# Kernel optimization log

Measured on AMD Instinct MI355X. Metric: run time of the kernel, lower is better.

The kernel has to match this reference:

```python
import jax, jax.numpy as jnp
import numpy as np

B, CQ, CC, COUT, H, W = 32, 256, 3, 256, 32, 32
INTER = CQ // 2
HC, WC = 224, 224
EPS = 1e-5


def setup_inputs() -> dict:
    key = jax.random.key(0)
    ks = jax.random.split(key, 12)
    s = lambda fan_in: 1.0 / np.sqrt(fan_in)
    return {
        "query_feat": jax.random.normal(ks[0], (B, CQ, H, W), jnp.float32),
        "context_feat": jax.random.normal(ks[1], (B, CC, HC, WC), jnp.float32),
        "Wq": jax.random.uniform(ks[2], (INTER, CQ), jnp.float32, -s(CQ), s(CQ)),
        "bq": jax.random.uniform(ks[3], (INTER,), jnp.float32, -s(CQ), s(CQ)),
        "Wk": jax.random.uniform(ks[4], (INTER, CC), jnp.float32, -s(CC), s(CC)),
        "bk": jax.random.uniform(ks[5], (INTER,), jnp.float32, -s(CC), s(CC)),
        "Wv": jax.random.uniform(ks[6], (CQ, CC), jnp.float32, -s(CC), s(CC)),
        "bv": jax.random.uniform(ks[7], (CQ,), jnp.float32, -s(CC), s(CC)),
        "Wp": jax.random.uniform(ks[8], (COUT, CQ), jnp.float32, -s(CQ), s(CQ)),
        "bp": jax.random.uniform(ks[9], (COUT,), jnp.float32, -s(CQ), s(CQ)),
        "gamma": jnp.ones((COUT,), jnp.float32),
        "beta": jnp.zeros((COUT,), jnp.float32),
    }


def _conv1x1(x, Wmat, b):
    # x: [B,Cin,H,W], Wmat: [Cout,Cin] -> [B,Cout,H,W]
    return jnp.einsum("oc,bchw->bohw", Wmat, x) + b[None, :, None, None]


def reference(query_feat, context_feat, Wq, bq, Wk, bk, Wv, bv, Wp, bp, gamma, beta):
    Bn, Cq, Hn, Wn = query_feat.shape
    HWn = Hn * Wn
    # bilinear resize, align_corners=False, no antialias (matches F.interpolate)
    ctx = jax.image.resize(context_feat, (Bn, context_feat.shape[1], Hn, Wn),
                           method="linear", antialias=False)
    q = _conv1x1(query_feat, Wq, bq).reshape(Bn, -1, HWn)   # [B,inter,HW]
    k = _conv1x1(ctx, Wk, bk).reshape(Bn, -1, HWn)          # [B,inter,HW]
    v = _conv1x1(ctx, Wv, bv).reshape(Bn, Cq, HWn)          # [B,Cq,HW]
    scores = jnp.einsum("bci,bcj->bij", q, k)               # [B,HW,HW]
    probs = jax.nn.softmax(scores, axis=-1)
    # attended_v[b,c,i] = sum_j v[b,c,j] * probs[b,i,j]
    attended = jnp.einsum("bcj,bij->bci", v, probs).reshape(Bn, Cq, Hn, Wn)
    fused = _conv1x1(query_feat + attended, Wp, bp)         # [B,Cout,H,W]
    # GroupNorm with 1 group: normalize over (C,H,W) per sample
    mu = jnp.mean(fused, axis=(1, 2, 3), keepdims=True)
    var = jnp.var(fused, axis=(1, 2, 3), keepdims=True)
    normed = (fused - mu) * jax.lax.rsqrt(var + EPS)
    return normed * gamma[None, :, None, None] + beta[None, :, None, None]
```

## Files before the change

kernel.cpp:

```cpp
#include <hip/hip_runtime.h>
#include <hip/hip_bf16.h>

#define WS_M     0
#define WS_G4    1024
#define WS_BSUM  2048
#define WS_BSSQ  2080
#define WS_WPB   2176

typedef __attribute__((ext_vector_type(8))) short short8;
typedef __attribute__((ext_vector_type(4))) float floatx4;

__device__ inline unsigned short f2bf(float x) {
    unsigned u = __float_as_uint(x);
    return (unsigned short)((u + 0x7FFFu + ((u >> 16) & 1u)) >> 16);
}

__global__ __launch_bounds__(256) void sca_pre(
    const float* __restrict__ Wq, const float* __restrict__ bq,
    const float* __restrict__ Wk, const float* __restrict__ bk,
    const float* __restrict__ Wv, const float* __restrict__ bv,
    const float* __restrict__ Wp, const float* __restrict__ bp,
    float* __restrict__ ws)
{
    int tid = threadIdx.x;
    int blk = blockIdx.x;
    if (blk == 0) {
        __shared__ float WkL[384];
        __shared__ float bqL[128];
        if (tid < 128) bqL[tid] = bq[tid];
        for (int idx = tid; idx < 384; idx += 256) WkL[idx] = Wk[idx];
        __syncthreads();
        float m0v = 0.f, m1v = 0.f, m2v = 0.f;
        for (int c0 = 0; c0 < 128; c0 += 16) {
            float q[16];
#pragma unroll
            for (int j = 0; j < 16; ++j) q[j] = Wq[(c0 + j) * 256 + tid];
#pragma unroll
            for (int j = 0; j < 16; ++j) {
                int c = c0 + j;
                m0v = fmaf(WkL[c * 3 + 0], q[j], m0v);
                m1v = fmaf(WkL[c * 3 + 1], q[j], m1v);
                m2v = fmaf(WkL[c * 3 + 2], q[j], m2v);
            }
        }
        ws[WS_M + 0   + tid] = m0v;
        ws[WS_M + 256 + tid] = m1v;
        ws[WS_M + 512 + tid] = m2v;
        if (tid < 3) {
            float s = 0.f;
            for (int c = 0; c < 128; ++c) s = fmaf(WkL[c * 3 + tid], bqL[c], s);
            ws[WS_M + 768 + tid] = s;
        }
        if (tid < 64) ws[WS_BSUM + tid] = 0.f;
    } else if (blk == 1) {
        __shared__ float WvL[768];
        __shared__ float bvL[256];
        for (int idx = tid; idx < 768; idx += 256) WvL[idx] = Wv[idx];
        bvL[tid] = bv[tid];
        __syncthreads();
        float g0 = 0.f, g1 = 0.f, g2 = 0.f, gb = 0.f;
        const float4* wr4 = (const float4*)(Wp + tid * 256);
        for (int c0 = 0; c0 < 64; c0 += 8) {
            float4 wv[8];
#pragma unroll
            for (int j = 0; j < 8; ++j) wv[j] = wr4[c0 + j];
#pragma unroll
            for (int j = 0; j < 8; ++j) {
                int c = (c0 + j) * 4;
                g0 = fmaf(wv[j].x, WvL[(c+0)*3+0], g0); g1 = fmaf(wv[j].x, WvL[(c+0)*3+1], g1); g2 = fmaf(wv[j].x, WvL[(c+0)*3+2], g2); gb = fmaf(wv[j].x, bvL[c+0], gb);
                g0 = fmaf(wv[j].y, WvL[(c+1)*3+0], g0); g1 = fmaf(wv[j].y, WvL[(c+1)*3+1], g1); g2 = fmaf(wv[j].y, WvL[(c+1)*3+2], g2); gb = fmaf(wv[j].y, bvL[c+1], gb);
                g0 = fmaf(wv[j].z, WvL[(c+2)*3+0], g0); g1 = fmaf(wv[j].z, WvL[(c+2)*3+1], g1); g2 = fmaf(wv[j].z, WvL[(c+2)*3+2], g2); gb = fmaf(wv[j].z, bvL[c+2], gb);
                g0 = fmaf(wv[j].w, WvL[(c+3)*3+0], g0); g1 = fmaf(wv[j].w, WvL[(c+3)*3+1], g1); g2 = fmaf(wv[j].w, WvL[(c+3)*3+2], g2); gb = fmaf(wv[j].w, bvL[c+3], gb);
            }
        }
        ((float4*)(ws + WS_G4))[tid] = make_float4(g0, g1, g2, gb + bp[tid]);
    } else {
        int idx = (blk - 2) * 2048 + tid * 8;
        int o = idx >> 8;
        int kt = (tid & 31) >> 2, quad = tid & 3;
        const float4* s = (const float4*)(Wp + idx);
        float4 x0 = s[0], x1 = s[1];
        uint4 v;
        v.x = (unsigned)f2bf(x0.x) | ((unsigned)f2bf(x0.y) << 16);
        v.y = (unsigned)f2bf(x0.z) | ((unsigned)f2bf(x0.w) << 16);
        v.z = (unsigned)f2bf(x1.x) | ((unsigned)f2bf(x1.y) << 16);
        v.w = (unsigned)f2bf(x1.z) | ((unsigned)f2bf(x1.w) << 16);
        int slot = (((o >> 4) * 8 + kt) * 64) + quad * 16 + (o & 15);
        ((uint4*)((unsigned short*)(ws + WS_WPB)))[slot] = v;
    }
}

__global__ __launch_bounds__(256, 2) void sca_fused(const float* __restrict__ Q,
                                                    const float* __restrict__ ctxin,
                                                    float* __restrict__ ws,
                                                    float* __restrict__ out)
{
    __shared__ float Ms[771];
    __shared__ float4 cs[1024];
    __shared__ uint4 QL[2048];
    __shared__ float red[4][16][12];
    __shared__ float4 av4[64];
    __shared__ float4 cps[64];
    int tid = threadIdx.x;
    int blk = blockIdx.x;
    int b  = blk >> 4;
    int i0 = (blk & 15) << 6;

    {
        const float* src = ctxin + (size_t)b * 150528;
        for (int s4 = 0; s4 < 4; ++s4) {
            int j = s4 * 256 + tid;
            int y = j >> 5, x = j & 31;
            int p = (7 * y + 3) * 224 + (7 * x + 3);
            cs[j] = make_float4(src[p], src[p + 50176], src[p + 100352], 0.f);
        }
    }
    for (int idx = tid; idx < 771; idx += 256) Ms[idx] = ws[WS_M + idx];
    __syncthreads();

    int iq = tid & 15, kg = tid >> 4;
    const float* Qp = Q + ((size_t)b << 18) + ((size_t)(kg * 16) << 10) + i0 + iq * 4;
    float a00=0.f,a01=0.f,a02=0.f,a03=0.f;
    float a10=0.f,a11=0.f,a12=0.f,a13=0.f;
    float a20=0.f,a21=0.f,a22=0.f,a23=0.f;
    unsigned pk[4][8];
#pragma unroll
    for (int s = 0; s < 16; ++s) {
        float4 qv = *(const float4*)(Qp + ((size_t)s << 10));
        int c = kg * 16 + s;
        float m0 = Ms[c], m1 = Ms[256 + c], m2 = Ms[512 + c];
        a00 = fmaf(m0, qv.x, a00); a01 = fmaf(m0, qv.y, a01); a02 = fmaf(m0, qv.z, a02); a03 = fmaf(m0, qv.w, a03);
        a10 = fmaf(m1, qv.x, a10); a11 = fmaf(m1, qv.y, a11); a12 = fmaf(m1, qv.z, a12); a13 = fmaf(m1, qv.w, a13);
        a20 = fmaf(m2, qv.x, a20); a21 = fmaf(m2, qv.y, a21); a22 = fmaf(m2, qv.z, a22); a23 = fmaf(m2, qv.w, a23);
        unsigned h0 = f2bf(qv.x), h1 = f2bf(qv.y), h2 = f2bf(qv.z), h3 = f2bf(qv.w);
        int j = s >> 1;
        if (s & 1) {
            pk[0][j] |= h0 << 16; pk[1][j] |= h1 << 16;
            pk[2][j] |= h2 << 16; pk[3][j] |= h3 << 16;
        } else {
            pk[0][j] = h0; pk[1][j] = h1; pk[2][j] = h2; pk[3][j] = h3;
        }
    }
#pragma unroll
    for (int e = 0; e < 4; ++e) {
        int row = iq * 4 + e;
        int sw = (row ^ (row >> 3)) & 7;
#pragma unroll
        for (int h = 0; h < 2; ++h) {
            int g = kg * 2 + h;
            int gs = (g & 24) | ((g ^ sw) & 7);
            QL[row * 32 + gs] =
                make_uint4(pk[e][h*4+0], pk[e][h*4+1], pk[e][h*4+2], pk[e][h*4+3]);
        }
    }
    a00 += __shfl_xor(a00,16); a00 += __shfl_xor(a00,32);
    a01 += __shfl_xor(a01,16); a01 += __shfl_xor(a01,32);
    a02 += __shfl_xor(a02,16); a02 += __shfl_xor(a02,32);
    a03 += __shfl_xor(a03,16); a03 += __shfl_xor(a03,32);
    a10 += __shfl_xor(a10,16); a10 += __shfl_xor(a10,32);
    a11 += __shfl_xor(a11,16); a11 += __shfl_xor(a11,32);
    a12 += __shfl_xor(a12,16); a12 += __shfl_xor(a12,32);
    a13 += __shfl_xor(a13,16); a13 += __shfl_xor(a13,32);
    a20 += __shfl_xor(a20,16); a20 += __shfl_xor(a20,32);
    a21 += __shfl_xor(a21,16); a21 += __shfl_xor(a21,32);
    a22 += __shfl_xor(a22,16); a22 += __shfl_xor(a22,32);
    a23 += __shfl_xor(a23,16); a23 += __shfl_xor(a23,32);
    int lane = tid & 63, w = tid >> 6;
    if (lane < 16) {
        red[w][lane][0]=a00; red[w][lane][1]=a01; red[w][lane][2] =a02; red[w][lane][3] =a03;
        red[w][lane][4]=a10; red[w][lane][5]=a11; red[w][lane][6] =a12; red[w][lane][7] =a13;
        red[w][lane][8]=a20; red[w][lane][9]=a21; red[w][lane][10]=a22; red[w][lane][11]=a23;
    }
    __syncthreads();
    if (tid < 64) {
        int iqq = tid >> 2, e = tid & 3;
        float r0 = red[0][iqq][0+e] + red[1][iqq][0+e] + red[2][iqq][0+e] + red[3][iqq][0+e] + Ms[768];
        float r1 = red[0][iqq][4+e] + red[1][iqq][4+e] + red[2][iqq][4+e] + red[3][iqq][4+e] + Ms[769];
        float r2 = red[0][iqq][8+e] + red[1][iqq][8+e] + red[2][iqq][8+e] + red[3][iqq][8+e] + Ms[770];
        av4[tid] = make_float4(r0, r1, r2, 0.f);
    }
    __syncthreads();

    int m = lane & 15, quad = lane >> 4;
    const short8* Apack = (const short8*)((const unsigned short*)(ws + WS_WPB));
    const short8* QLs = (const short8*)QL;
    floatx4 acc[4][4] = {};
#pragma unroll
    for (int kt = 0; kt < 8; ++kt) {
        short8 af[4], bf[4];
#pragma unroll
        for (int t = 0; t < 4; ++t)
            af[t] = Apack[((w * 4 + t) * 8 + kt) * 64 + lane];
#pragma unroll
        for (int t = 0; t < 4; ++t) {
            int row = t * 16 + m;
            int sw = (row ^ (row >> 3)) & 7;
            int g = kt * 4 + quad;
            int gs = (g & 24) | ((g ^ sw) & 7);
            bf[t] = QLs[row * 32 + gs];
        }
#pragma unroll
        for (int to = 0; to < 4; ++to)
#pragma unroll
            for (int ti = 0; ti < 4; ++ti)
                acc[to][ti] = __builtin_amdgcn_mfma_f32_16x16x32_bf16(
                    af[to], bf[ti], acc[to][ti], 0, 0, 0);
    }

    {
        int qi = tid >> 2, sl = tid & 3;
        float4 a = av4[qi];
        float sh = 6.0f * (fabsf(a.x) + fabsf(a.y) + fabsf(a.z));
        float d = 0.f, s0 = 0.f, s1 = 0.f, s2 = 0.f;
#pragma unroll 4
        for (int jj = 0; jj < 256; ++jj) {
            float4 c = cs[(jj << 2) + sl];
            float sc = fmaf(a.x, c.x, fmaf(a.y, c.y, a.z * c.z));
            float e = __expf(sc - sh);
            d += e;
            s0 = fmaf(e, c.x, s0);
            s1 = fmaf(e, c.y, s1);
            s2 = fmaf(e, c.z, s2);
        }
        d  += __shfl_xor(d, 1);  d  += __shfl_xor(d, 2);
        s0 += __shfl_xor(s0, 1); s0 += __shfl_xor(s0, 2);
        s1 += __shfl_xor(s1, 1); s1 += __shfl_xor(s1, 2);
        s2 += __shfl_xor(s2, 1); s2 += __shfl_xor(s2, 2);
        if (sl == 0) {
            float inv = 1.0f / d;
            cps[qi] = make_float4(s0 * inv, s1 * inv, s2 * inv, 0.f);
        }
    }
    __syncthreads();

    const floatx4* G4 = (const floatx4*)(ws + WS_G4);
    float4 cpv[4];
#pragma unroll
    for (int ti = 0; ti < 4; ++ti) cpv[ti] = cps[ti * 16 + m];
    float lsum = 0.f, lssq = 0.f;
#pragma unroll
    for (int to = 0; to < 4; ++to)
#pragma unroll
        for (int r = 0; r < 4; ++r) {
            int o = w * 64 + to * 16 + quad * 4 + r;
            floatx4 g = G4[o];
            float* orow = out + (((size_t)(b * 256 + o)) << 10) + i0 + m;
#pragma unroll
            for (int ti = 0; ti < 4; ++ti) {
                float v = acc[to][ti][r]
                        + g[0] * cpv[ti].x + g[1] * cpv[ti].y + g[2] * cpv[ti].z + g[3];
                orow[ti * 16] = v;
                lsum += v; lssq = fmaf(v, v, lssq);
            }
        }
#pragma unroll
    for (int off = 32; off > 0; off >>= 1) {
        lsum += __shfl_down(lsum, off);
        lssq += __shfl_down(lssq, off);
    }
    if (lane == 0) {
        atomicAdd(ws + WS_BSUM + b, lsum);
        atomicAdd(ws + WS_BSSQ + b, lssq);
    }
}

__global__ __launch_bounds__(256) void sca_norm(float* __restrict__ out,
                                                const float* __restrict__ ws,
                                                const float* __restrict__ gamma,
                                                const float* __restrict__ beta)
{
    size_t idx = (size_t)blockIdx.x * 256 + threadIdx.x;
    float4 v = ((const float4*)out)[idx];
    size_t base = idx << 2;
    int b = (int)(base >> 18);
    int o = (int)((base >> 10) & 255);
    const float inv_n = 1.0f / 262144.0f;
    float mean = ws[WS_BSUM + b] * inv_n;
    float var  = fmaf(ws[WS_BSSQ + b], inv_n, -mean * mean);
    float rs = rsqrtf(var + 1e-5f);
    float ga = gamma[o] * rs;
    float be = fmaf(-mean, ga, beta[o]);
    v.x = fmaf(v.x, ga, be);
    v.y = fmaf(v.y, ga, be);
    v.z = fmaf(v.z, ga, be);
    v.w = fmaf(v.w, ga, be);
    ((float4*)out)[idx] = v;
}

extern "C" void kernel_launch(void* const* d_in, const int* in_sizes, int n_in,
                              void* d_out, int out_size, void* d_ws, size_t ws_size,
                              hipStream_t stream)
{
    const float* Q     = (const float*)d_in[0];
    const float* ctxf  = (const float*)d_in[1];
    const float* Wq    = (const float*)d_in[2];
    const float* bq    = (const float*)d_in[3];
    const float* Wk    = (const float*)d_in[4];
    const float* bk    = (const float*)d_in[5];
    const float* Wv    = (const float*)d_in[6];
    const float* bv    = (const float*)d_in[7];
    const float* Wp    = (const float*)d_in[8];
    const float* bp    = (const float*)d_in[9];
    const float* gamma = (const float*)d_in[10];
    const float* beta  = (const float*)d_in[11];
    float* ws  = (float*)d_ws;
    float* out = (float*)d_out;

    sca_pre  <<<34,   256, 0, stream>>>(Wq, bq, Wk, bk, Wv, bv, Wp, bp, ws);
    sca_fused<<<512,  256, 0, stream>>>(Q, ctxf, ws, out);
    sca_norm <<<8192, 256, 0, stream>>>(out, ws, gamma, beta);
}
```

Baseline: 173.1 us.

## Parallelize precompute, hoist context gather into pre-kernel, raise fused occupancy

The weight precompute in sca_pre is split across more blocks. The M matrix reduction runs over 4 blocks with shared-memory partial sums, and the G4 projection is folded into the 32 Wp conversion blocks using shuffle reductions. The strided context-subsample gather moves into 128 extra sca_pre blocks that write a compact float4 buffer, so each of the 16 fused blocks per batch no longer re-gathers it with uncoalesced loads. sca_fused switches its context tile to SoA arrays, reuses the red buffer for cps, and targets 3 blocks per CU. sca_norm processes 4 float4s per thread with fewer blocks.

```diff
diff --git a/kernel.cpp b/kernel.cpp
--- a/kernel.cpp
+++ b/kernel.cpp
@@ -6,6 +6,7 @@
 #define WS_BSUM  2048
 #define WS_BSSQ  2080
 #define WS_WPB   2176
+#define WS_CTX   34944
 
 typedef __attribute__((ext_vector_type(8))) short short8;
 typedef __attribute__((ext_vector_type(4))) float floatx4;
@@ -20,21 +21,24 @@
     const float* __restrict__ Wk, const float* __restrict__ bk,
     const float* __restrict__ Wv, const float* __restrict__ bv,
     const float* __restrict__ Wp, const float* __restrict__ bp,
-    float* __restrict__ ws)
+    const float* __restrict__ ctxin, float* __restrict__ ws)
 {
     int tid = threadIdx.x;
     int blk = blockIdx.x;
-    if (blk == 0) {
+    if (blk < 4) {
         __shared__ float WkL[384];
         __shared__ float bqL[128];
+        __shared__ float redM[4][64][3];
+        int o0 = blk << 6;
         if (tid < 128) bqL[tid] = bq[tid];
         for (int idx = tid; idx < 384; idx += 256) WkL[idx] = Wk[idx];
         __syncthreads();
+        int o64 = tid & 63, cg = tid >> 6;
         float m0v = 0.f, m1v = 0.f, m2v = 0.f;
-        for (int c0 = 0; c0 < 128; c0 += 16) {
+        for (int c0 = cg * 32; c0 < cg * 32 + 32; c0 += 16) {
             float q[16];
 #pragma unroll
-            for (int j = 0; j < 16; ++j) q[j] = Wq[(c0 + j) * 256 + tid];
+            for (int j = 0; j < 16; ++j) q[j] = Wq[(c0 + j) * 256 + o0 + o64];
 #pragma unroll
             for (int j = 0; j < 16; ++j) {
                 int c = c0 + j;
@@ -43,39 +47,31 @@
                 m2v = fmaf(WkL[c * 3 + 2], q[j], m2v);
             }
         }
-        ws[WS_M + 0   + tid] = m0v;
-        ws[WS_M + 256 + tid] = m1v;
-        ws[WS_M + 512 + tid] = m2v;
-        if (tid < 3) {
-            float s = 0.f;
-            for (int c = 0; c < 128; ++c) s = fmaf(WkL[c * 3 + tid], bqL[c], s);
-            ws[WS_M + 768 + tid] = s;
-        }
-        if (tid < 64) ws[WS_BSUM + tid] = 0.f;
-    } else if (blk == 1) {
+        redM[cg][o64][0] = m0v; redM[cg][o64][1] = m1v; redM[cg][o64][2] = m2v;
+        __syncthreads();
+        if (tid < 64) {
+            float r0 = redM[0][tid][0] + redM[1][tid][0] + redM[2][tid][0] + redM[3][tid][0];
+            float r1 = redM[0][tid][1] + redM[1][tid][1] + redM[2][tid][1] + redM[3][tid][1];
+            float r2 = redM[0][tid][2] + redM[1][tid][2] + redM[2][tid][2] + redM[3][tid][2];
+            ws[WS_M + 0   + o0 + tid] = r0;
+            ws[WS_M + 256 + o0 + tid] = r1;
+            ws[WS_M + 512 + o0 + tid] = r2;
+        }
+        if (blk == 0) {
+            if (tid < 3) {
+                float s = 0.f;
+                for (int c = 0; c < 128; ++c) s = fmaf(WkL[c * 3 + tid], bqL[c], s);
+                ws[WS_M + 768 + tid] = s;
+            }
+            if (tid < 64) ws[WS_BSUM + tid] = 0.f;
+        }
+    } else if (blk < 36) {
         __shared__ float WvL[768];
         __shared__ float bvL[256];
         for (int idx = tid; idx < 768; idx += 256) WvL[idx] = Wv[idx];
         bvL[tid] = bv[tid];
         __syncthreads();
-        float g0 = 0.f, g1 = 0.f, g2 = 0.f, gb = 0.f;
-        const float4* wr4 = (const float4*)(Wp + tid * 256);
-        for (int c0 = 0; c0 < 64; c0 += 8) {
-            float4 wv[8];
-#pragma unroll
-            for (int j = 0; j < 8; ++j) wv[j] = wr4[c0 + j];
-#pragma unroll
-            for (int j = 0; j < 8; ++j) {
-                int c = (c0 + j) * 4;
-                g0 = fmaf(wv[j].x, WvL[(c+0)*3+0], g0); g1 = fmaf(wv[j].x, WvL[(c+0)*3+1], g1); g2 = fmaf(wv[j].x, WvL[(c+0)*3+2], g2); gb = fmaf(wv[j].x, bvL[c+0], gb);
-                g0 = fmaf(wv[j].y, WvL[(c+1)*3+0], g0); g1 = fmaf(wv[j].y, WvL[(c+1)*3+1], g1); g2 = fmaf(wv[j].y, WvL[(c+1)*3+2], g2); gb = fmaf(wv[j].y, bvL[c+1], gb);
-                g0 = fmaf(wv[j].z, WvL[(c+2)*3+0], g0); g1 = fmaf(wv[j].z, WvL[(c+2)*3+1], g1); g2 = fmaf(wv[j].z, WvL[(c+2)*3+2], g2); gb = fmaf(wv[j].z, bvL[c+2], gb);
-                g0 = fmaf(wv[j].w, WvL[(c+3)*3+0], g0); g1 = fmaf(wv[j].w, WvL[(c+3)*3+1], g1); g2 = fmaf(wv[j].w, WvL[(c+3)*3+2], g2); gb = fmaf(wv[j].w, bvL[c+3], gb);
-            }
-        }
-        ((float4*)(ws + WS_G4))[tid] = make_float4(g0, g1, g2, gb + bp[tid]);
-    } else {
-        int idx = (blk - 2) * 2048 + tid * 8;
+        int idx = (blk - 4) * 2048 + tid * 8;
         int o = idx >> 8;
         int kt = (tid & 31) >> 2, quad = tid & 3;
         const float4* s = (const float4*)(Wp + idx);
@@ -87,32 +83,62 @@
         v.w = (unsigned)f2bf(x1.z) | ((unsigned)f2bf(x1.w) << 16);
         int slot = (((o >> 4) * 8 + kt) * 64) + quad * 16 + (o & 15);
         ((uint4*)((unsigned short*)(ws + WS_WPB)))[slot] = v;
-    }
-}
-
-__global__ __launch_bounds__(256, 2) void sca_fused(const float* __restrict__ Q,
-                                                    const float* __restrict__ ctxin,
+        int c0 = idx & 255;
+        float xv[8] = {x0.x, x0.y, x0.z, x0.w, x1.x, x1.y, x1.z, x1.w};
+        float g0 = 0.f, g1 = 0.f, g2 = 0.f, gb = 0.f;
+#pragma unroll
+        for (int j = 0; j < 8; ++j) {
+            int c = c0 + j;
+            g0 = fmaf(xv[j], WvL[c * 3 + 0], g0);
+            g1 = fmaf(xv[j], WvL[c * 3 + 1], g1);
+            g2 = fmaf(xv[j], WvL[c * 3 + 2], g2);
+            gb = fmaf(xv[j], bvL[c], gb);
+        }
+#pragma unroll
+        for (int off = 1; off < 32; off <<= 1) {
+            g0 += __shfl_xor(g0, off);
+            g1 += __shfl_xor(g1, off);
+            g2 += __shfl_xor(g2, off);
+            gb += __shfl_xor(gb, off);
+        }
+        if ((tid & 31) == 0)
+            ((float4*)(ws + WS_G4))[o] = make_float4(g0, g1, g2, gb + bp[o]);
+    } else {
+        int g = (blk - 36) * 256 + tid;
+        int b = g >> 10, j = g & 1023;
+        int y = j >> 5, x = j & 31;
+        const float* src = ctxin + (size_t)b * 150528;
+        int p = (7 * y + 3) * 224 + (7 * x + 3);
+        ((float4*)(ws + WS_CTX))[g] =
+            make_float4(src[p], src[p + 50176], src[p + 100352], 0.f);
+    }
+}
+
+__global__ __launch_bounds__(256, 3) void sca_fused(const float* __restrict__ Q,
                                                     float* __restrict__ ws,
                                                     float* __restrict__ out)
 {
     __shared__ float Ms[771];
-    __shared__ float4 cs[1024];
+    __shared__ float cs0[1024];
+    __shared__ float cs1[1024];
+    __shared__ float cs2[1024];
     __shared__ uint4 QL[2048];
     __shared__ float red[4][16][12];
     __shared__ float4 av4[64];
-    __shared__ float4 cps[64];
+    float4* cps = (float4*)red;
+
     int tid = threadIdx.x;
     int blk = blockIdx.x;
     int b  = blk >> 4;
     int i0 = (blk & 15) << 6;
 
     {
-        const float* src = ctxin + (size_t)b * 150528;
+        const float4* cg4 = ((const float4*)(ws + WS_CTX)) + ((size_t)b << 10);
+#pragma unroll
         for (int s4 = 0; s4 < 4; ++s4) {
             int j = s4 * 256 + tid;
-            int y = j >> 5, x = j & 31;
-            int p = (7 * y + 3) * 224 + (7 * x + 3);
-            cs[j] = make_float4(src[p], src[p + 50176], src[p + 100352], 0.f);
+            float4 v = cg4[j];
+            cs0[j] = v.x; cs1[j] = v.y; cs2[j] = v.z;
         }
     }
     for (int idx = tid; idx < 771; idx += 256) Ms[idx] = ws[WS_M + idx];
@@ -214,13 +240,14 @@
         float d = 0.f, s0 = 0.f, s1 = 0.f, s2 = 0.f;
 #pragma unroll 4
         for (int jj = 0; jj < 256; ++jj) {
-            float4 c = cs[(jj << 2) + sl];
-            float sc = fmaf(a.x, c.x, fmaf(a.y, c.y, a.z * c.z));
+            int j = (jj << 2) + sl;
+            float c0 = cs0[j], c1 = cs1[j], c2 = cs2[j];
+            float sc = fmaf(a.x, c0, fmaf(a.y, c1, a.z * c2));
             float e = __expf(sc - sh);
             d += e;
-            s0 = fmaf(e, c.x, s0);
-            s1 = fmaf(e, c.y, s1);
-            s2 = fmaf(e, c.z, s2);
+            s0 = fmaf(e, c0, s0);
+            s1 = fmaf(e, c1, s1);
+            s2 = fmaf(e, c2, s2);
         }
         d  += __shfl_xor(d, 1);  d  += __shfl_xor(d, 2);
         s0 += __shfl_xor(s0, 1); s0 += __shfl_xor(s0, 2);
@@ -269,22 +296,25 @@
                                                 const float* __restrict__ gamma,
                                                 const float* __restrict__ beta)
 {
-    size_t idx = (size_t)blockIdx.x * 256 + threadIdx.x;
-    float4 v = ((const float4*)out)[idx];
-    size_t base = idx << 2;
-    int b = (int)(base >> 18);
-    int o = (int)((base >> 10) & 255);
     const float inv_n = 1.0f / 262144.0f;
-    float mean = ws[WS_BSUM + b] * inv_n;
-    float var  = fmaf(ws[WS_BSSQ + b], inv_n, -mean * mean);
-    float rs = rsqrtf(var + 1e-5f);
-    float ga = gamma[o] * rs;
-    float be = fmaf(-mean, ga, beta[o]);
-    v.x = fmaf(v.x, ga, be);
-    v.y = fmaf(v.y, ga, be);
-    v.z = fmaf(v.z, ga, be);
-    v.w = fmaf(v.w, ga, be);
-    ((float4*)out)[idx] = v;
+#pragma unroll
+    for (int r = 0; r < 4; ++r) {
+        size_t idx = (size_t)r * 524288 + (size_t)blockIdx.x * 256 + threadIdx.x;
+        float4 v = ((const float4*)out)[idx];
+        size_t base = idx << 2;
+        int b = (int)(base >> 18);
+        int o = (int)((base >> 10) & 255);
+        float mean = ws[WS_BSUM + b] * inv_n;
+        float var  = fmaf(ws[WS_BSSQ + b], inv_n, -mean * mean);
+        float rs = rsqrtf(var + 1e-5f);
+        float ga = gamma[o] * rs;
+        float be = fmaf(-mean, ga, beta[o]);
+        v.x = fmaf(v.x, ga, be);
+        v.y = fmaf(v.y, ga, be);
+        v.z = fmaf(v.z, ga, be);
+        v.w = fmaf(v.w, ga, be);
+        ((float4*)out)[idx] = v;
+    }
 }
 
 extern "C" void kernel_launch(void* const* d_in, const int* in_sizes, int n_in,
@@ -306,7 +336,7 @@
     float* ws  = (float*)d_ws;
     float* out = (float*)d_out;
 
-    sca_pre  <<<34,   256, 0, stream>>>(Wq, bq, Wk, bk, Wv, bv, Wp, bp, ws);
-    sca_fused<<<512,  256, 0, stream>>>(Q, ctxf, ws, out);
-    sca_norm <<<8192, 256, 0, stream>>>(out, ws, gamma, beta);
-}
+    sca_pre  <<<164,  256, 0, stream>>>(Wq, bq, Wk, bk, Wv, bv, Wp, bp, ctxf, ws);
+    sca_fused<<<512,  256, 0, stream>>>(Q, ws, out);
+    sca_norm <<<2048, 256, 0, stream>>>(out, ws, gamma, beta);
+}
```

After: 165.6 us. 1.04x faster.
